# Performance work log

Measured on AMD Instinct MI355X. Metric: run time of the kernel, lower is better.

Reference implementation:

```python
import jax, jax.numpy as jnp
import numpy as np

NUM_CAPS = 2          # NUM_CLASSES
R = 16 * 10 * 10 * 10 # num_route_nodes = 16000
NUM_ITERS = 3


def conv3d(x, w, b, stride):
    y = jax.lax.conv_general_dilated(
        x, w, window_strides=(stride, stride, stride), padding='VALID',
        dimension_numbers=('NCDHW', 'OIDHW', 'NCDHW'))
    return y + b[None, :, None, None, None]


def squash(t, axis=-1):
    n = jnp.linalg.norm(t, axis=axis, keepdims=True)
    scale = n ** 2 / (1 + n ** 2) / (n + 1e-8)
    return scale * t


def setup_inputs() -> dict:
    key = jax.random.key(0)
    ks = jax.random.split(key, 16)
    inp = {
        'x': jax.random.normal(ks[0], (16, 1, 29, 29, 29), jnp.float32),
        'conv1_w': 0.05 * jax.random.normal(ks[1], (128, 1, 3, 3, 3), jnp.float32),
        'conv1_b': jnp.zeros((128,), jnp.float32),
        # 8 primary capsules, each Conv3d(128,16,k=9,s=2), stacked cap-major
        'pcaps_w': 0.01 * jax.random.normal(ks[2], (8 * 16, 128, 9, 9, 9), jnp.float32),
        'pcaps_b': jnp.zeros((8 * 16,), jnp.float32),
        'route_w': 0.01 * jax.random.normal(ks[3], (NUM_CAPS, R, 8, 16), jnp.float32),
        'dec_w1': 0.05 * jax.random.normal(ks[4], (32, 512), jnp.float32),
        'dec_b1': jnp.zeros((512,), jnp.float32),
        'dec_w2': 0.05 * jax.random.normal(ks[5], (512, 2048), jnp.float32),
        'dec_b2': jnp.zeros((2048,), jnp.float32),
        'dec_w3': 0.02 * jax.random.normal(ks[6], (2048, 10240), jnp.float32),
        'dec_b3': jnp.zeros((10240,), jnp.float32),
        'dec_w4': 0.02 * jax.random.normal(ks[7], (10240, 27000), jnp.float32),
        'dec_b4': jnp.zeros((27000,), jnp.float32),
    }
    return inp


def reference(x, conv1_w, conv1_b, pcaps_w, pcaps_b, route_w,
              dec_w1, dec_b1, dec_w2, dec_b2, dec_w3, dec_b3, dec_w4, dec_b4):
    B = x.shape[0]
    # stem conv + relu: [B,128,27,27,27]
    h = jax.nn.relu(conv3d(x, conv1_w, conv1_b, 1))
    # primary capsules (8 convs fused into one): [B,128,10,10,10]
    p = conv3d(h, pcaps_w, pcaps_b, 2)
    # torch: per-capsule view(B,-1,1) then cat dim=-1 -> [B,16000,8]
    p = p.reshape(B, 8, R).transpose(0, 2, 1)
    u = squash(p, axis=-1)  # [B,R,8]

    # priors: x[:,None,:,None,:] @ W[None] -> [B,C,R,16] (singleton dim dropped)
    priors = jnp.einsum('bri,crio->bcro', u, route_w)
    priors_d = jax.lax.stop_gradient(priors)
    # torch logits have trailing dim 16 but are constant along it (delta is
    # broadcast), so [B,C,R,1] is mathematically identical.
    logits = jnp.zeros((B, NUM_CAPS, R, 1), priors.dtype)

    for i in range(NUM_ITERS):
        probs = jax.nn.softmax(logits, axis=1)  # over capsule axis
        if i == NUM_ITERS - 1:
            v = squash((probs * priors).sum(axis=2, keepdims=True))
        else:
            v = squash((probs * priors_d).sum(axis=2, keepdims=True))
            logits = logits + (priors_d * v).sum(axis=-1, keepdims=True)

    caps = v[:, :, 0, :]  # [B,C,16] (squeeze)
    classes = jnp.linalg.norm(caps, axis=-1)  # [B,C]

    # y=None branch: one-hot of argmax
    y = jax.nn.one_hot(jnp.argmax(classes, axis=1), NUM_CAPS, dtype=caps.dtype)
    d = (caps * y[:, :, None]).reshape(B, -1)  # [B,32]
    d = jax.nn.relu(d @ dec_w1 + dec_b1)
    d = jax.nn.relu(d @ dec_w2 + dec_b2)
    d = jax.nn.relu(d @ dec_w3 + dec_b3)
    recon = jax.nn.sigmoid(d @ dec_w4 + dec_b4)  # [B,27000]
    return classes, recon
```

## Files before the change

### kernel.cpp

```cpp
#include <hip/hip_runtime.h>
#include <hip/hip_bf16.h>

#define NB   16
#define XS   29
#define HS   27
#define HSP  19683
#define PSP  1000
#define RR   16000
#define KTAP 729
#define SPTOT 314928

#define HT_SLOT   81648UL
#define HT_TOTAL  41803776UL
#define HT_PLANE  3024
#define W2B_CH    4096
#define W2B_ICG   376832UL

#define OFF_WT   0UL
#define OFF_H    11943936UL
#define OFF_SP   52254720UL
#define OFF_U    54302720UL
#define OFF_PRI  56350720UL
#define OFF_LOG  64542720UL
#define OFF_V    65055232UL
#define OFF_D0   65055744UL
#define OFF_D1   65056256UL
#define OFF_D2   65064448UL
#define OFF_D3   65097216UL
#define OFF_PP   65693056UL
#define OFF_D3P  82077056UL
#define OFF_D4P  87319936UL
#define OFF_D2P  91610496UL
#undef  OFF_D2P
#define OFF_D2P  101143936UL

typedef __attribute__((ext_vector_type(8))) short bf16x8;
typedef __attribute__((ext_vector_type(4))) float f32x4;

#define GL2LDS16(g, l) __builtin_amdgcn_global_load_lds( \
    (const __attribute__((address_space(1))) void*)(g), \
    (__attribute__((address_space(3))) void*)(l), 16, 0, 0)

__global__ void prep_w2b(const float* __restrict__ w, ushort* __restrict__ w2b) {
    int gid = blockIdx.x * 256 + threadIdx.x;
    int oc  = gid / 11776;
    int r   = gid % 11776;
    int icg = r / 368;
    int r2  = r % 368;
    int c = r2 >> 2, kq = r2 & 3;
    const float* wb = w + (size_t)oc * 93312 + (size_t)icg * 4 * KTAP;
    ushort vals[8];
    #pragma unroll
    for (int j = 0; j < 8; j++) {
        int ic = j & 3, half = j >> 2;
        float v = 0.f;
        if (c < 81) {
            int tap = c * 9 + 2 * kq + half;
            v = wb[ic * KTAP + tap];
        } else {
            int dzy = (c - 81) * 8 + 2 * kq + half;
            if (dzy <= 80) v = wb[ic * KTAP + dzy * 9 + 8];
        }
        __hip_bfloat16 hv = __float2bfloat16(v);
        vals[j] = *(ushort*)&hv;
    }
    ushort* dst = w2b + ((size_t)((icg * 92 + c) * 4 + kq) * 128 + oc) * 8;
    #pragma unroll
    for (int j = 0; j < 8; j++) dst[j] = vals[j];
}

__global__ __launch_bounds__(256) void conv1_relu_t(const float* __restrict__ x,
                                                    const float* __restrict__ w,
                                                    const float* __restrict__ bias,
                                                    ushort* __restrict__ hT) {
    __shared__ ushort lt[32][132];
    int t = threadIdx.x;
    int c = t & 127;
    float wr[27];
    #pragma unroll
    for (int k = 0; k < 27; k++) wr[k] = w[c * 27 + k];
    float bv = bias[c];
    int sp0 = blockIdx.x * 32;
    #pragma unroll 4
    for (int i = 0; i < 16; i++) {
        int spl = i * 2 + (t >> 7);
        int spg = sp0 + spl;
        if (spg < SPTOT) {
            int b = spg / HSP, sp = spg % HSP;
            int z = sp / 729, y = (sp / 27) % 27, xx = sp % 27;
            const float* xb = x + (size_t)b * (XS * XS * XS) + ((size_t)z * XS + y) * XS + xx;
            float xv[27];
            #pragma unroll
            for (int dz = 0; dz < 3; dz++)
                #pragma unroll
                for (int dy = 0; dy < 3; dy++)
                    #pragma unroll
                    for (int dx = 0; dx < 3; dx++)
                        xv[(dz * 3 + dy) * 3 + dx] = xb[((size_t)dz * XS + dy) * XS + dx];
            float acc = bv;
            #pragma unroll
            for (int k = 0; k < 27; k++) acc = fmaf(xv[k], wr[k], acc);
            __hip_bfloat16 hv = __float2bfloat16(fmaxf(acc, 0.f));
            lt[spl][c] = *(ushort*)&hv;
        }
    }
    __syncthreads();
    #pragma unroll
    for (int q = 0; q < 4; q++) {
        int gidx = q * 256 + t;
        int icg = gidx >> 5, spl = gidx & 31;
        int spg = sp0 + spl;
        if (spg < SPTOT) {
            int b = spg / HSP, sp = spg % HSP;
            int z = sp / 729, y = (sp / 27) % 27, xx = sp % 27;
            *(short4*)(hT + (size_t)(icg * 16 + b) * HT_SLOT
                          + ((size_t)(z * 27 + y) * 28 + xx) * 4) =
                *(const short4*)&lt[spl][icg * 4];
        }
    }
}

__global__ __launch_bounds__(512, 4) void pcaps_conv(const ushort* __restrict__ hT,
                                                     const ushort* __restrict__ w2b,
                                                     float* __restrict__ pp) {
    __shared__ __align__(16) ushort AT[36288];
    int t = threadIdx.x;
    int bid = blockIdx.x;
    int g = bid & 7;
    int rest = bid >> 3;
    int b = rest / 5, ozt = rest % 5;
    int z0 = ozt * 4;

    int lane = t & 63, wave = t >> 6;
    int ocb = wave * 16;
    int l15 = lane & 15, kq = lane >> 4;

    int vox[13];
    #pragma unroll
    for (int f = 0; f < 13; f++) {
        int lr = f * 16 + l15; if (lr > 199) lr = 199;
        int ozl = lr / 100; int rem = lr % 100;
        int oy = rem / 10, ox = rem % 10;
        vox[f] = (2 * ozl) * 6048 + (2 * oy) * 224 + (2 * ox) * 8;
    }

    f32x4 acc[13];
    #pragma unroll
    for (int f = 0; f < 13; f++) acc[f] = (f32x4)0.f;

    int bvoff = (kq * 128 + ocb + l15) * 8;

    for (int ph = 0; ph < 4; ++ph) {
        int icg = g * 4 + ph;
        const ushort* src = hT + (size_t)(icg * 16 + b) * HT_SLOT + (size_t)z0 * HT_PLANE;
        if (ph) __syncthreads();
        #pragma unroll
        for (int q = 0; q < 9; q++) {
            int gi = q * 512 + t;
            if (gi < 4536)
                GL2LDS16(src + (size_t)gi * 8, AT + (size_t)gi * 8);
        }
        asm volatile("s_waitcnt vmcnt(0)" ::: "memory");
        __syncthreads();

        const ushort* wB = w2b + (size_t)icg * W2B_ICG;
        bf16x8 bv = *(const bf16x8*)(wB + bvoff);
        for (int c = 0; c < 81; ++c) {
            bf16x8 bvn = *(const bf16x8*)(wB + (size_t)(c + 1) * W2B_CH + bvoff);
            int coff = (c / 9) * 6048 + (c % 9) * 224 + kq * 16;
            #pragma unroll
            for (int f = 0; f < 13; f++) {
                bf16x8 av = *(const bf16x8*)((const char*)AT + vox[f] + coff);
                acc[f] = __builtin_amdgcn_mfma_f32_16x16x32_bf16(av, bv, acc[f], 0, 0, 0);
            }
            bv = bvn;
        }
        for (int cc = 0; cc < 11; ++cc) {
            int nxt = (cc == 10) ? 91 : 82 + cc;
            bf16x8 bvn = *(const bf16x8*)(wB + (size_t)nxt * W2B_CH + bvoff);
            int dzy0 = cc * 8 + 2 * kq;
            int dzy1 = dzy0 + 1;
            int o0 = (dzy0 / 9) * 6048 + (dzy0 % 9) * 224 + 64;
            int o1 = (dzy1 / 9) * 6048 + (dzy1 % 9) * 224 + 64;
            #pragma unroll
            for (int f = 0; f < 13; f++) {
                union { bf16x8 v; short4 h[2]; } a;
                a.h[0] = *(const short4*)((const char*)AT + vox[f] + o0);
                a.h[1] = *(const short4*)((const char*)AT + vox[f] + o1);
                acc[f] = __builtin_amdgcn_mfma_f32_16x16x32_bf16(a.v, bv, acc[f], 0, 0, 0);
            }
            bv = bvn;
        }
    }

    float* pg = pp + (size_t)g * 2048000;
    int mbase = b * 1000 + ozt * 200;
    #pragma unroll
    for (int f = 0; f < 13; f++) {
        #pragma unroll
        for (int r = 0; r < 4; r++) {
            int lr = f * 16 + kq * 4 + r;
            if (lr < 200)
                pg[(size_t)(mbase + lr) * 128 + ocb + l15] = acc[f][r];
        }
    }
}

__global__ void squash_red(const float* __restrict__ pp, const float* __restrict__ pb,
                           float* __restrict__ u) {
    __shared__ float rowv[2][128];
    int t = threadIdx.x;
    int m = blockIdx.x * 2 + (t >> 7);
    int ch = t & 127;
    float v = pb[ch];
    #pragma unroll
    for (int g = 0; g < 8; g++) v += pp[(size_t)g * 2048000 + (size_t)m * 128 + ch];
    rowv[t >> 7][ch] = v;
    __syncthreads();
    if (t < 32) {
        int row = t >> 4, rq = t & 15;
        int mm = blockIdx.x * 2 + row;
        int b = mm / PSP, s = mm % PSP;
        float vals[8], ss = 0.f;
        #pragma unroll
        for (int i = 0; i < 8; i++) { float x = rowv[row][i * 16 + rq]; vals[i] = x; ss += x * x; }
        float n = sqrtf(ss);
        float sc = ss / (1.f + ss) / (n + 1e-8f);
        float* dst = u + ((size_t)b * RR + rq * 1000 + s) * 8;
        #pragma unroll
        for (int i = 0; i < 8; i++) dst[i] = vals[i] * sc;
    }
}

__global__ void priors_k(const float* __restrict__ u, const float* __restrict__ rw,
                         float* __restrict__ pri) {
    __shared__ float wl[16][132];
    int bx = blockIdx.x; int c = bx / 1000; int r0 = (bx % 1000) * 16;
    int t = threadIdx.x;
    const float4* src = (const float4*)(rw + ((size_t)c * RR + r0) * 128);
    #pragma unroll
    for (int q = 0; q < 8; q++) {
        int idx = q * 256 + t;
        int row = idx >> 5, c4 = idx & 31;
        *(float4*)&wl[row][c4 * 4] = src[idx];
    }
    __syncthreads();
    int bb = t >> 4, rl = t & 15;
    const float* up = u + ((size_t)bb * RR + r0 + rl) * 8;
    float4 u0 = *(const float4*)up, u1 = *(const float4*)(up + 4);
    float uu[8] = {u0.x, u0.y, u0.z, u0.w, u1.x, u1.y, u1.z, u1.w};
    float out[16];
    #pragma unroll
    for (int o = 0; o < 16; o++) out[o] = 0.f;
    #pragma unroll
    for (int i = 0; i < 8; i++)
        #pragma unroll
        for (int o = 0; o < 16; o++) out[o] += uu[i] * wl[rl][i * 16 + o];
    float* dst = pri + ((size_t)(bb * 2 + c) * RR + r0 + rl) * 16;
    #pragma unroll
    for (int q = 0; q < 4; q++)
        *(float4*)&dst[q * 4] = make_float4(out[q*4], out[q*4+1], out[q*4+2], out[q*4+3]);
}

__global__ void route_s0(const float* __restrict__ pri, float* __restrict__ spart) {
    int b = blockIdx.x, chunk = blockIdx.y;
    int t = threadIdx.x, o = t & 15, rl = t >> 4;
    float acc0 = 0.f, acc1 = 0.f;
    for (int j = 0; j < 40; j++) {
        int r = chunk * 640 + j * 16 + rl;
        acc0 += pri[((size_t)(b * 2 + 0) * RR + r) * 16 + o];
        acc1 += pri[((size_t)(b * 2 + 1) * RR + r) * 16 + o];
    }
    __shared__ float red[2][16][17];
    red[0][rl][o] = acc0; red[1][rl][o] = acc1;
    __syncthreads();
    for (int step = 8; step >= 1; step >>= 1) {
        if (rl < step) {
            red[0][rl][o] += red[0][rl + step][o];
            red[1][rl][o] += red[1][rl + step][o];
        }
        __syncthreads();
    }
    if (rl == 0) {
        spart[((b * 25 + chunk) * 2 + 0) * 16 + o] = 0.5f * red[0][0][o];
        spart[((b * 25 + chunk) * 2 + 1) * 16 + o] = 0.5f * red[1][0][o];
    }
}

template<int MODE>
__global__ void route_iter(const float* __restrict__ pri, const float* __restrict__ v,
                           float* __restrict__ lg, float* __restrict__ spart) {
    int b = blockIdx.x, chunk = blockIdx.y;
    int t = threadIdx.x, o = t & 15, rl = t >> 4;
    float v0 = v[(b * 2 + 0) * 16 + o], v1 = v[(b * 2 + 1) * 16 + o];
    float acc0 = 0.f, acc1 = 0.f;
    for (int j = 0; j < 40; j++) {
        int r = chunk * 640 + j * 16 + rl;
        float p0 = pri[((size_t)(b * 2 + 0) * RR + r) * 16 + o];
        float p1 = pri[((size_t)(b * 2 + 1) * RR + r) * 16 + o];
        float d0 = p0 * v0, d1 = p1 * v1;
        #pragma unroll
        for (int w = 1; w < 16; w <<= 1) { d0 += __shfl_xor(d0, w); d1 += __shfl_xor(d1, w); }
        float l0, l1;
        if (MODE == 1) {
            l0 = d0; l1 = d1;
            if (o == 0) lg[(size_t)(b * 2 + 0) * RR + r] = d0;
            if (o == 1) lg[(size_t)(b * 2 + 1) * RR + r] = d1;
        } else {
            l0 = lg[(size_t)(b * 2 + 0) * RR + r] + d0;
            l1 = lg[(size_t)(b * 2 + 1) * RR + r] + d1;
        }
        float mx = fmaxf(l0, l1);
        float e0 = __expf(l0 - mx), e1 = __expf(l1 - mx);
        float inv = 1.f / (e0 + e1);
        acc0 += (e0 * inv) * p0;
        acc1 += (e1 * inv) * p1;
    }
    __shared__ float red[2][16][17];
    red[0][rl][o] = acc0; red[1][rl][o] = acc1;
    __syncthreads();
    for (int step = 8; step >= 1; step >>= 1) {
        if (rl < step) {
            red[0][rl][o] += red[0][rl + step][o];
            red[1][rl][o] += red[1][rl + step][o];
        }
        __syncthreads();
    }
    if (rl == 0) {
        spart[((b * 25 + chunk) * 2 + 0) * 16 + o] = red[0][0][o];
        spart[((b * 25 + chunk) * 2 + 1) * 16 + o] = red[1][0][o];
    }
}

__global__ void squash_v_parts(const float* __restrict__ spart, float* __restrict__ v) {
    int t = threadIdx.x;
    int bc = t >> 4, o = t & 15;
    int b = bc >> 1, c = bc & 1;
    float x = 0.f;
    for (int ch = 0; ch < 25; ch++) x += spart[((b * 25 + ch) * 2 + c) * 16 + o];
    __shared__ float sv[32][17];
    sv[bc][o] = x;
    __syncthreads();
    float ss = 0.f;
    #pragma unroll
    for (int i = 0; i < 16; i++) { float y = sv[bc][i]; ss += y * y; }
    float n = sqrtf(ss);
    float sc = ss / (1.f + ss) / (n + 1e-8f);
    v[bc * 16 + o] = x * sc;
}

__global__ void squash_v_cls(const float* __restrict__ spart, float* __restrict__ out,
                             float* __restrict__ d0) {
    int t = threadIdx.x;
    int bc = t >> 4, o = t & 15;
    int b = bc >> 1, c = bc & 1;
    float x = 0.f;
    for (int ch = 0; ch < 25; ch++) x += spart[((b * 25 + ch) * 2 + c) * 16 + o];
    __shared__ float sv[32][17];
    __shared__ float vv[32][17];
    __shared__ float cls[32];
    sv[bc][o] = x;
    __syncthreads();
    float ss = 0.f;
    #pragma unroll
    for (int i = 0; i < 16; i++) { float y = sv[bc][i]; ss += y * y; }
    float n = sqrtf(ss);
    float sc = ss / (1.f + ss) / (n + 1e-8f);
    vv[bc][o] = x * sc;
    __syncthreads();
    if (t < 32) {
        float s2 = 0.f;
        #pragma unroll
        for (int i = 0; i < 16; i++) { float y = vv[t][i]; s2 += y * y; }
        float nn = sqrtf(s2);
        cls[t] = nn; out[t] = nn;
    }
    __syncthreads();
    int bb = t >> 5, k = t & 31, cc = k >> 4;
    int win = (cls[bb * 2 + 1] > cls[bb * 2 + 0]) ? 1 : 0;
    d0[t] = (cc == win) ? vv[bb * 2 + cc][k & 15] : 0.f;
}

template<int K>
__global__ void dec_small(const float* __restrict__ din, const float* __restrict__ W,
                          const float* __restrict__ bias, float* __restrict__ dout, int N) {
    __shared__ float dl[16 * K];
    int t = threadIdx.x;
    for (int i = t; i < 16 * K; i += 256) dl[i] = din[i];
    __syncthreads();
    int n = blockIdx.x * 256 + t;
    if (n >= N) return;
    float acc[16];
    float bv = bias[n];
    #pragma unroll
    for (int b = 0; b < 16; b++) acc[b] = bv;
    for (int k = 0; k < K; k++) {
        float w = W[(size_t)k * N + n];
        #pragma unroll
        for (int b = 0; b < 16; b++) acc[b] += dl[b * K + k] * w;
    }
    #pragma unroll
    for (int b = 0; b < 16; b++) dout[(size_t)b * N + n] = fmaxf(acc[b], 0.f);
}

__global__ void dec_small_split(const float* __restrict__ din, const float* __restrict__ W,
                                float* __restrict__ part) {
    __shared__ float dl[16 * 64];
    int t = threadIdx.x;
    int ks = blockIdx.y;
    for (int i = t; i < 16 * 64; i += 256) {
        int b = i >> 6, kk = i & 63;
        dl[i] = din[b * 512 + ks * 64 + kk];
    }
    __syncthreads();
    int n = blockIdx.x * 256 + t;
    float acc[16];
    #pragma unroll
    for (int b = 0; b < 16; b++) acc[b] = 0.f;
    for (int kk = 0; kk < 64; kk++) {
        float w = W[(size_t)(ks * 64 + kk) * 2048 + n];
        #pragma unroll
        for (int b = 0; b < 16; b++) acc[b] += dl[b * 64 + kk] * w;
    }
    #pragma unroll
    for (int b = 0; b < 16; b++)
        part[((size_t)(ks * 16 + b)) * 2048 + n] = acc[b];
}

__global__ void dec_split(const float* __restrict__ din, const float* __restrict__ W,
                          float* __restrict__ part, int N, int K, int KC) {
    extern __shared__ float dl[];
    int t = threadIdx.x;
    int ky = blockIdx.y;
    int k0 = ky * KC;
    for (int i = t; i < 16 * KC; i += 256) {
        int b = i / KC, kk = i % KC;
        dl[i] = din[(size_t)b * K + k0 + kk];
    }
    __syncthreads();
    int n = blockIdx.x * 1024 + t * 4;
    if (n >= N) return;
    float4 acc[16];
    #pragma unroll
    for (int b = 0; b < 16; b++) acc[b] = make_float4(0.f, 0.f, 0.f, 0.f);
    const float* Wp = W + (size_t)k0 * N + n;
    for (int kk = 0; kk < KC; kk++) {
        float4 w = *(const float4*)&Wp[(size_t)kk * N];
        #pragma unroll
        for (int b = 0; b < 16; b++) {
            float dv = dl[b * KC + kk];
            acc[b].x += dv * w.x; acc[b].y += dv * w.y;
            acc[b].z += dv * w.z; acc[b].w += dv * w.w;
        }
    }
    #pragma unroll
    for (int b = 0; b < 16; b++)
        *(float4*)&part[((size_t)(ky * 16 + b)) * N + n] = acc[b];
}

__global__ void bias_act_sum(const float* __restrict__ part, const float* __restrict__ bias,
                             float* __restrict__ out, int N, int total, int sigm, int KY) {
    int gid = blockIdx.x * 256 + threadIdx.x;
    if (gid >= total) return;
    int b = gid / N, n = gid % N;
    float x = bias[n];
    for (int ky = 0; ky < KY; ky++)
        x += part[((size_t)(ky * 16 + b)) * N + n];
    out[gid] = sigm ? (1.f / (1.f + __expf(-x))) : fmaxf(x, 0.f);
}

extern "C" void kernel_launch(void* const* d_in, const int* in_sizes, int n_in,
                              void* d_out, int out_size, void* d_ws, size_t ws_size,
                              hipStream_t stream) {
    const float* x        = (const float*)d_in[0];
    const float* conv1_w  = (const float*)d_in[1];
    const float* conv1_b  = (const float*)d_in[2];
    const float* pcaps_w  = (const float*)d_in[3];
    const float* pcaps_b  = (const float*)d_in[4];
    const float* route_w  = (const float*)d_in[5];
    const float* dec_w1   = (const float*)d_in[6];
    const float* dec_b1   = (const float*)d_in[7];
    const float* dec_w2   = (const float*)d_in[8];
    const float* dec_b2   = (const float*)d_in[9];
    const float* dec_w3   = (const float*)d_in[10];
    const float* dec_b3   = (const float*)d_in[11];
    const float* dec_w4   = (const float*)d_in[12];
    const float* dec_b4   = (const float*)d_in[13];
    float* out = (float*)d_out;

    float* ws = (float*)d_ws;
    ushort* w2b = (ushort*)(ws + OFF_WT);
    ushort* hT  = (ushort*)(ws + OFF_H);
    float* spart = ws + OFF_SP;
    float* u    = ws + OFF_U;
    float* pri  = ws + OFF_PRI;
    float* lg   = ws + OFF_LOG;
    float* v    = ws + OFF_V;
    float* d0   = ws + OFF_D0;
    float* d1   = ws + OFF_D1;
    float* d2   = ws + OFF_D2;
    float* d3   = ws + OFF_D3;
    float* pp   = ws + OFF_PP;
    float* d3p  = ws + OFF_D3P;
    float* d4p  = ws + OFF_D4P;
    float* d2p  = ws + OFF_D2P;

    prep_w2b<<<5888, 256, 0, stream>>>(pcaps_w, w2b);
    conv1_relu_t<<<9842, 256, 0, stream>>>(x, conv1_w, conv1_b, hT);
    hipMemsetAsync(hT + HT_TOTAL, 0, 8192, stream);

    pcaps_conv<<<640, 512, 0, stream>>>(hT, w2b, pp);
    squash_red<<<8000, 256, 0, stream>>>(pp, pcaps_b, u);

    priors_k<<<2000, 256, 0, stream>>>(u, route_w, pri);

    route_s0<<<dim3(16, 25), 256, 0, stream>>>(pri, spart);
    squash_v_parts<<<1, 512, 0, stream>>>(spart, v);
    route_iter<1><<<dim3(16, 25), 256, 0, stream>>>(pri, v, lg, spart);
    squash_v_parts<<<1, 512, 0, stream>>>(spart, v);
    route_iter<2><<<dim3(16, 25), 256, 0, stream>>>(pri, v, lg, spart);
    squash_v_cls<<<1, 512, 0, stream>>>(spart, out, d0);

    dec_small<32><<<2, 256, 0, stream>>>(d0, dec_w1, dec_b1, d1, 512);
    dec_small_split<<<dim3(8, 8), 256, 0, stream>>>(d1, dec_w2, d2p);
    bias_act_sum<<<(16 * 2048 + 255) / 256, 256, 0, stream>>>(d2p, dec_b2, d2, 2048, 16 * 2048, 0, 8);

    dec_split<<<dim3(10, 32), 256, 16 * 64 * sizeof(float), stream>>>(d2, dec_w3, d3p, 10240, 2048, 64);
    bias_act_sum<<<(16 * 10240 + 255) / 256, 256, 0, stream>>>(d3p, dec_b3, d3, 10240, 16 * 10240, 0, 32);

    dec_split<<<dim3(27, 32), 256, 16 * 320 * sizeof(float), stream>>>(d3, dec_w4, d4p, 27000, 10240, 320);
    bias_act_sum<<<(16 * 27000 + 255) / 256, 256, 0, stream>>>(d4p, dec_b4, out + 32, 27000, 16 * 27000, 1, 32);
}
```

Before: 1.053 ms.

## Switch primary-capsule conv to 32x32x16 MFMA with new weight layout

Rewrites the pcaps implicit-GEMM conv to use 32x32x16 bf16 MFMA tiles instead of 16x16x32. The weight prep kernel emits a new chunked layout to match. Each wave now covers 32 output channels and half of the 200 voxel rows, using 4 (or 3) 16-wide accumulators in place of 13 4-wide ones. The aim is fewer LDS A-fragment reads per FLOP and fewer, larger MFMA issues, at the cost of uneven work between the wave halves and twice as many K-chunks per phase.

```diff
diff --git a/kernel.cpp b/kernel.cpp
--- a/kernel.cpp
+++ b/kernel.cpp
@@ -13,8 +13,8 @@
 #define HT_SLOT   81648UL
 #define HT_TOTAL  41803776UL
 #define HT_PLANE  3024
-#define W2B_CH    4096
-#define W2B_ICG   376832UL
+#define W2C_CH    2048
+#define W2C_ICG   374784UL
 
 #define OFF_WT   0UL
 #define OFF_H    11943936UL
@@ -30,41 +30,44 @@
 #define OFF_PP   65693056UL
 #define OFF_D3P  82077056UL
 #define OFF_D4P  87319936UL
-#define OFF_D2P  91610496UL
-#undef  OFF_D2P
 #define OFF_D2P  101143936UL
 
 typedef __attribute__((ext_vector_type(8))) short bf16x8;
 typedef __attribute__((ext_vector_type(4))) float f32x4;
+typedef __attribute__((ext_vector_type(16))) float f32x16;
 
 #define GL2LDS16(g, l) __builtin_amdgcn_global_load_lds( \
     (const __attribute__((address_space(1))) void*)(g), \
     (__attribute__((address_space(3))) void*)(l), 16, 0, 0)
 
-__global__ void prep_w2b(const float* __restrict__ w, ushort* __restrict__ w2b) {
+__global__ void prep_w2c(const float* __restrict__ w, ushort* __restrict__ w2c) {
     int gid = blockIdx.x * 256 + threadIdx.x;
-    int oc  = gid / 11776;
-    int r   = gid % 11776;
-    int icg = r / 368;
-    int r2  = r % 368;
-    int c = r2 >> 2, kq = r2 & 3;
+    int icg = gid / 46848;
+    int r   = gid % 46848;
+    int chunk = r / 256;
+    int r2  = r % 256;
+    int ocg = r2 >> 6, lane = r2 & 63;
+    int h = lane >> 5, col = lane & 31;
+    int oc = ocg * 32 + col;
     const float* wb = w + (size_t)oc * 93312 + (size_t)icg * 4 * KTAP;
     ushort vals[8];
     #pragma unroll
     for (int j = 0; j < 8; j++) {
-        int ic = j & 3, half = j >> 2;
+        int ic = j & 3;
         float v = 0.f;
-        if (c < 81) {
-            int tap = c * 9 + 2 * kq + half;
-            v = wb[ic * KTAP + tap];
+        if (chunk < 162) {
+            int dzdy = chunk >> 1, d0 = (chunk & 1) * 4;
+            int dx = d0 + 2 * h + (j >> 2);
+            v = wb[ic * KTAP + dzdy * 9 + dx];
         } else {
-            int dzy = (c - 81) * 8 + 2 * kq + half;
+            int dzy = (chunk - 162) * 4 + 2 * h + (j >> 2);
             if (dzy <= 80) v = wb[ic * KTAP + dzy * 9 + 8];
         }
         __hip_bfloat16 hv = __float2bfloat16(v);
         vals[j] = *(ushort*)&hv;
     }
-    ushort* dst = w2b + ((size_t)((icg * 92 + c) * 4 + kq) * 128 + oc) * 8;
+    ushort* dst = w2c + (size_t)icg * W2C_ICG + (size_t)chunk * W2C_CH
+                      + (size_t)(ocg * 64 + lane) * 8;
     #pragma unroll
     for (int j = 0; j < 8; j++) dst[j] = vals[j];
 }
@@ -121,7 +124,7 @@
 }
 
 __global__ __launch_bounds__(512, 4) void pcaps_conv(const ushort* __restrict__ hT,
-                                                     const ushort* __restrict__ w2b,
+                                                     const ushort* __restrict__ w2c,
                                                      float* __restrict__ pp) {
     __shared__ __align__(16) ushort AT[36288];
     int t = threadIdx.x;
@@ -132,23 +135,22 @@
     int z0 = ozt * 4;
 
     int lane = t & 63, wave = t >> 6;
-    int ocb = wave * 16;
-    int l15 = lane & 15, kq = lane >> 4;
-
-    int vox[13];
-    #pragma unroll
-    for (int f = 0; f < 13; f++) {
-        int lr = f * 16 + l15; if (lr > 199) lr = 199;
-        int ozl = lr / 100; int rem = lr % 100;
+    int ocg = wave >> 1, fh = wave & 1;
+    int NF = 4 - fh;
+    int col = lane & 31, h = lane >> 5;
+
+    int vox[4];
+    #pragma unroll
+    for (int fi = 0; fi < 4; fi++) {
+        int r = (fh * 4 + fi) * 32 + col; if (r > 199) r = 199;
+        int ozl = r / 100; int rem = r % 100;
         int oy = rem / 10, ox = rem % 10;
-        vox[f] = (2 * ozl) * 6048 + (2 * oy) * 224 + (2 * ox) * 8;
-    }
-
-    f32x4 acc[13];
-    #pragma unroll
-    for (int f = 0; f < 13; f++) acc[f] = (f32x4)0.f;
-
-    int bvoff = (kq * 128 + ocb + l15) * 8;
+        vox[fi] = (2 * ozl) * 6048 + (2 * oy) * 224 + (2 * ox) * 8;
+    }
+
+    f32x16 acc[4];
+    #pragma unroll
+    for (int fi = 0; fi < 4; fi++) acc[fi] = (f32x16)0.f;
 
     for (int ph = 0; ph < 4; ++ph) {
         int icg = g * 4 + ph;
@@ -163,31 +165,36 @@
         asm volatile("s_waitcnt vmcnt(0)" ::: "memory");
         __syncthreads();
 
-        const ushort* wB = w2b + (size_t)icg * W2B_ICG;
-        bf16x8 bv = *(const bf16x8*)(wB + bvoff);
-        for (int c = 0; c < 81; ++c) {
-            bf16x8 bvn = *(const bf16x8*)(wB + (size_t)(c + 1) * W2B_CH + bvoff);
-            int coff = (c / 9) * 6048 + (c % 9) * 224 + kq * 16;
+        const ushort* wB = w2c + (size_t)icg * W2C_ICG + (size_t)(ocg * 64 + lane) * 8;
+        bf16x8 bv = *(const bf16x8*)wB;
+        for (int c = 0; c < 162; ++c) {
+            bf16x8 bvn = *(const bf16x8*)(wB + (size_t)(c + 1) * W2C_CH);
+            int dzdy = c >> 1, d0 = (c & 1) * 4;
+            int coff = (dzdy / 9) * 6048 + (dzdy % 9) * 224 + (d0 + 2 * h) * 8;
             #pragma unroll
-            for (int f = 0; f < 13; f++) {
-                bf16x8 av = *(const bf16x8*)((const char*)AT + vox[f] + coff);
-                acc[f] = __builtin_amdgcn_mfma_f32_16x16x32_bf16(av, bv, acc[f], 0, 0, 0);
+            for (int fi = 0; fi < 4; fi++) {
+                if (fi < NF) {
+                    bf16x8 av = *(const bf16x8*)((const char*)AT + vox[fi] + coff);
+                    acc[fi] = __builtin_amdgcn_mfma_f32_32x32x16_bf16(av, bv, acc[fi], 0, 0, 0);
+                }
             }
             bv = bvn;
         }
-        for (int cc = 0; cc < 11; ++cc) {
-            int nxt = (cc == 10) ? 91 : 82 + cc;
-            bf16x8 bvn = *(const bf16x8*)(wB + (size_t)nxt * W2B_CH + bvoff);
-            int dzy0 = cc * 8 + 2 * kq;
+        for (int cidx = 162; cidx < 183; ++cidx) {
+            bf16x8 bvn = *(const bf16x8*)(wB + (size_t)((cidx + 1 < 183) ? cidx + 1 : cidx) * W2C_CH);
+            int dzq = cidx - 162;
+            int dzy0 = dzq * 4 + 2 * h;
             int dzy1 = dzy0 + 1;
             int o0 = (dzy0 / 9) * 6048 + (dzy0 % 9) * 224 + 64;
             int o1 = (dzy1 / 9) * 6048 + (dzy1 % 9) * 224 + 64;
             #pragma unroll
-            for (int f = 0; f < 13; f++) {
-                union { bf16x8 v; short4 h[2]; } a;
-                a.h[0] = *(const short4*)((const char*)AT + vox[f] + o0);
-                a.h[1] = *(const short4*)((const char*)AT + vox[f] + o1);
-                acc[f] = __builtin_amdgcn_mfma_f32_16x16x32_bf16(a.v, bv, acc[f], 0, 0, 0);
+            for (int fi = 0; fi < 4; fi++) {
+                if (fi < NF) {
+                    union { bf16x8 v; short4 s4[2]; } a;
+                    a.s4[0] = *(const short4*)((const char*)AT + vox[fi] + o0);
+                    a.s4[1] = *(const short4*)((const char*)AT + vox[fi] + o1);
+                    acc[fi] = __builtin_amdgcn_mfma_f32_32x32x16_bf16(a.v, bv, acc[fi], 0, 0, 0);
+                }
             }
             bv = bvn;
         }
@@ -196,12 +203,16 @@
     float* pg = pp + (size_t)g * 2048000;
     int mbase = b * 1000 + ozt * 200;
     #pragma unroll
-    for (int f = 0; f < 13; f++) {
-        #pragma unroll
-        for (int r = 0; r < 4; r++) {
-            int lr = f * 16 + kq * 4 + r;
-            if (lr < 200)
-                pg[(size_t)(mbase + lr) * 128 + ocb + l15] = acc[f][r];
+    for (int fi = 0; fi < 4; fi++) {
+        if (fi < NF) {
+            int f = fh * 4 + fi;
+            #pragma unroll
+            for (int reg = 0; reg < 16; reg++) {
+                int row32 = (reg & 3) + 8 * (reg >> 2) + 4 * h;
+                int lr = f * 32 + row32;
+                if (lr < 200)
+                    pg[(size_t)(mbase + lr) * 128 + ocg * 32 + col] = acc[fi][reg];
+            }
         }
     }
 }
@@ -489,7 +500,7 @@
     float* out = (float*)d_out;
 
     float* ws = (float*)d_ws;
-    ushort* w2b = (ushort*)(ws + OFF_WT);
+    ushort* w2c = (ushort*)(ws + OFF_WT);
     ushort* hT  = (ushort*)(ws + OFF_H);
     float* spart = ws + OFF_SP;
     float* u    = ws + OFF_U;
@@ -505,11 +516,11 @@
     float* d4p  = ws + OFF_D4P;
     float* d2p  = ws + OFF_D2P;
 
-    prep_w2b<<<5888, 256, 0, stream>>>(pcaps_w, w2b);
+    prep_w2c<<<5856, 256, 0, stream>>>(pcaps_w, w2c);
     conv1_relu_t<<<9842, 256, 0, stream>>>(x, conv1_w, conv1_b, hT);
     hipMemsetAsync(hT + HT_TOTAL, 0, 8192, stream);
 
-    pcaps_conv<<<640, 512, 0, stream>>>(hT, w2b, pp);
+    pcaps_conv<<<640, 512, 0, stream>>>(hT, w2c, pp);
     squash_red<<<8000, 256, 0, stream>>>(pp, pcaps_b, u);
 
     priors_k<<<2000, 256, 0, stream>>>(u, route_w, pri);
```

Result: slower. 1.109 ms (+5.3%).
